# Kernel tuning notes

Measured on AMD Instinct MI355X. Metric: run time of the kernel, lower is better.

Reference implementation:

```python
import jax, jax.numpy as jnp
import numpy as np

N_PARENT = 16384
N_CHILD = 8 * N_PARENT  # nearest upsample, nempty=False: 8 children per parent
C = 128
K = 27  # 3x3x3 octree conv stencil


def setup_inputs() -> dict:
    key = jax.random.key(0)
    k1, k2, k3, k4 = jax.random.split(key, 4)
    x = jax.random.normal(k1, (N_PARENT, C), dtype=jnp.float32)
    # conv weight per stencil offset, fan-in scaled init
    w = jax.random.normal(k2, (K, C, C), dtype=jnp.float32) / np.sqrt(K * C)
    b = jnp.zeros((C,), dtype=jnp.float32)
    # neighbor table at depth+1; -1 marks missing neighbors (zero-padded)
    neigh = jax.random.randint(k3, (N_CHILD, K), -1, N_CHILD, dtype=jnp.int32)
    return {"x": x, "w": w, "b": b, "neigh": neigh}


def reference(x, w, b, neigh):
    # OctreeUpsample(nearest, nempty=False): copy each parent feature to its
    # 8 contiguous children at depth+1.
    xu = jnp.repeat(x, 8, axis=0)  # [N_child, C]
    # OctreeConv: gather 27 neighbors (missing -> 0), then GEMM + bias.
    valid = neigh >= 0  # [N_child, 27]
    g = jnp.where(valid[..., None], xu[jnp.clip(neigh, 0)], 0.0)  # [N_child, 27, C]
    out = jnp.einsum('nkc,kcd->nd', g, w) + b  # [N_child, C]
    return out
```

## Files before the change

kernel.cpp:

```cpp
#include <hip/hip_runtime.h>
#include <hip/hip_bf16.h>

#define N_PARENT 16384
#define N_CHILD (8 * N_PARENT)
#define CC 128
#define KK 27

#define BM 128
#define BN 128
#define BK 32

#define XB_OFF 0
#define XB_ELEMS (N_PARENT * CC)
#define WT_OFF XB_ELEMS
#define WT_ELEMS (KK * CC * CC)
#define ZR_OFF (WT_OFF + WT_ELEMS)
#define ZR_ELEMS 128
#define ZR_ROW 19840

typedef __attribute__((ext_vector_type(8))) __bf16 bf16x8;
typedef __attribute__((ext_vector_type(4))) float f32x4;

__device__ __forceinline__ void gll16(const void* g, void* l) {
  __builtin_amdgcn_global_load_lds(
      (const __attribute__((address_space(1))) unsigned int*)g,
      (__attribute__((address_space(3))) unsigned int*)l,
      16, 0, 0);
}

__global__ void prep_kernel(const float* __restrict__ x,
                            const float* __restrict__ w,
                            __hip_bfloat16* __restrict__ ws) {
  const int stride = gridDim.x * blockDim.x;
  const int tid = blockIdx.x * blockDim.x + threadIdx.x;
  for (int i = tid; i < XB_ELEMS; i += stride)
    ws[XB_OFF + i] = __float2bfloat16(x[i]);
  for (int j = tid; j < WT_ELEMS; j += stride) {
    const int k = j / (CC * CC);
    const int rem = j - k * CC * CC;
    const int d = rem >> 7;
    const int c = rem & 127;
    ws[WT_OFF + j] = __float2bfloat16(w[k * CC * CC + c * CC + d]);
  }
  if (tid < ZR_ELEMS) ws[ZR_OFF + tid] = __float2bfloat16(0.0f);
}

__global__ __launch_bounds__(256, 4) void upconv_kernel(
    const int* __restrict__ neigh,
    const __hip_bfloat16* __restrict__ ws,
    const float* __restrict__ bias,
    float* __restrict__ out) {
  __shared__ __align__(16) __hip_bfloat16 As[2][BM * BK];
  __shared__ __align__(16) __hip_bfloat16 Bs[2][BN * BK];
  __shared__ unsigned short ridx[BM * KK];

  const int tid = threadIdx.x;
  const int wv = tid >> 6;
  const int l = tid & 63;
  const int wr = wv >> 1;
  const int wc = wv & 1;
  const int row0 = blockIdx.x * BM;

  for (int j = tid; j < BM * KK; j += 256) {
    const int nv = neigh[row0 * KK + j];
    ridx[j] = (unsigned short)((nv >= 0) ? (nv >> 3) : ZR_ROW);
  }
  __syncthreads();

  const int lr = l & 15;
  const int lk8 = (l >> 4) * 8;
  const int g16 = l >> 2;
  const int lbA = (l & 3) * 16;
  const int sB = g16 * 256 + lbA;

  const char* xbB = (const char*)(ws + XB_OFF);
  const char* wp = (const char*)(ws + WT_OFF);

  f32x4 acc[4][4] = {};

  const int ri0 = (wv * 32 + g16) * KK;
  const int ri1 = (wv * 32 + 16 + g16) * KK;
  int r0 = ((int)ridx[ri0]) << 8;
  int r1 = ((int)ridx[ri1]) << 8;

  auto stageA = [&](int buf, int qb, int a0, int a1) {
    gll16(xbB + a0 + qb + lbA, &As[buf][(wv * 32) * BK]);
    gll16(xbB + a1 + qb + lbA, &As[buf][(wv * 32 + 16) * BK]);
  };
  auto stageB = [&](int buf, const char* w, int qb) {
    gll16(w + (wv * 32) * 256 + qb + sB, &Bs[buf][(wv * 32) * BK]);
    gll16(w + (wv * 32 + 16) * 256 + qb + sB, &Bs[buf][(wv * 32 + 16) * BK]);
  };

  auto compute = [&](int buf) {
    bf16x8 a[4], b[4];
#pragma unroll
    for (int m = 0; m < 4; ++m)
      a[m] = *reinterpret_cast<const bf16x8*>(
          &As[buf][(wr * 64 + m * 16 + lr) * BK + lk8]);
#pragma unroll
    for (int n = 0; n < 4; ++n)
      b[n] = *reinterpret_cast<const bf16x8*>(
          &Bs[buf][(wc * 64 + n * 16 + lr) * BK + lk8]);
    __builtin_amdgcn_s_setprio(1);
#pragma unroll
    for (int m = 0; m < 4; ++m)
#pragma unroll
      for (int n = 0; n < 4; ++n)
        acc[m][n] = __builtin_amdgcn_mfma_f32_16x16x32_bf16(
            a[m], b[n], acc[m][n], 0, 0, 0);
    __builtin_amdgcn_s_setprio(0);
  };

#define WAITN(n) asm volatile("s_waitcnt vmcnt(" #n ")" ::: "memory")
#define BAR() __builtin_amdgcn_s_barrier()

  stageB(0, wp, 0);
  stageA(0, 0, r0, r1);

  for (int k = 0; k < KK; ++k) {
    stageB(1, wp, 64);
    stageA(1, 64, r0, r1);
    WAITN(4); BAR();
    compute(0);
    BAR();

    stageB(0, wp, 128);
    stageA(0, 128, r0, r1);
    WAITN(4); BAR();
    compute(1);
    BAR();

    stageB(1, wp, 192);
    stageA(1, 192, r0, r1);
    int n0 = r0, n1 = r1;
    if (k + 1 < KK) {
      n0 = ((int)ridx[ri0 + k + 1]) << 8;
      n1 = ((int)ridx[ri1 + k + 1]) << 8;
    }
    WAITN(4); BAR();
    compute(0);
    BAR();

    wp += 2 * CC * CC;
    if (k + 1 < KK) {
      stageB(0, wp, 0);
      stageA(0, 0, n0, n1);
      WAITN(4);
    } else {
      WAITN(0);
    }
    BAR();
    compute(1);
    BAR();

    r0 = n0; r1 = n1;
  }

  float bv[4];
#pragma unroll
  for (int n = 0; n < 4; ++n) bv[n] = bias[wc * 64 + n * 16 + lr];
  const int rbase = row0 + wr * 64 + (l >> 4) * 4;
#pragma unroll
  for (int m = 0; m < 4; ++m)
#pragma unroll
    for (int n = 0; n < 4; ++n)
#pragma unroll
      for (int q = 0; q < 4; ++q)
        out[(size_t)(rbase + m * 16 + q) * CC + wc * 64 + n * 16 + lr] =
            acc[m][n][q] + bv[n];
}

extern "C" void kernel_launch(void* const* d_in, const int* in_sizes, int n_in,
                              void* d_out, int out_size, void* d_ws,
                              size_t ws_size, hipStream_t stream) {
  const float* x = (const float*)d_in[0];
  const float* w = (const float*)d_in[1];
  const float* b = (const float*)d_in[2];
  const int* neigh = (const int*)d_in[3];
  __hip_bfloat16* ws = (__hip_bfloat16*)d_ws;
  float* out = (float*)d_out;

  hipLaunchKernelGGL(prep_kernel, dim3(512), dim3(256), 0, stream, x, w, ws);
  hipLaunchKernelGGL(upconv_kernel, dim3(N_CHILD / BM), dim3(256), 0, stream,
                     neigh, ws, b, out);
}
```

Measured before the change: 152.2 us.

## Double M tile to 256 rows and XOR-swizzle LDS layout for gathers

Doubles the block's row tile from 128 to 256 so each wave holds a 128x64 accumulator (8x4 MFMA tiles), which halves the weight-tile loads per output row. Adds an XOR swizzle to both the global-to-LDS load lane offsets and the LDS fragment reads, intended to cut LDS bank conflicts. The vmcnt waits are adjusted to match the six async loads now issued per stage. In exchange, register pressure roughly doubles, launch bounds drop to 2 blocks per SM, and the grid halves, which lowers occupancy and reduces the number of blocks available to fill the CUs.

```diff
diff --git a/kernel.cpp b/kernel.cpp
--- a/kernel.cpp
+++ b/kernel.cpp
@@ -6,7 +6,7 @@
 #define CC 128
 #define KK 27
 
-#define BM 128
+#define BM 256
 #define BN 128
 #define BK 32
 
@@ -45,7 +45,7 @@
   if (tid < ZR_ELEMS) ws[ZR_OFF + tid] = __float2bfloat16(0.0f);
 }
 
-__global__ __launch_bounds__(256, 4) void upconv_kernel(
+__global__ __launch_bounds__(256, 2) void upconv_kernel(
     const int* __restrict__ neigh,
     const __hip_bfloat16* __restrict__ ws,
     const float* __restrict__ bias,
@@ -68,43 +68,44 @@
   __syncthreads();
 
   const int lr = l & 15;
-  const int lk8 = (l >> 4) * 8;
-  const int g16 = l >> 2;
-  const int lbA = (l & 3) * 16;
-  const int sB = g16 * 256 + lbA;
+  const int coE = (((l >> 4) ^ ((lr >> 1) & 3)) * 8);
+  const int lch = ((l & 3) ^ ((l >> 3) & 3)) * 16;
 
   const char* xbB = (const char*)(ws + XB_OFF);
-  const char* wp = (const char*)(ws + WT_OFF);
+  const char* wLane =
+      (const char*)(ws + WT_OFF) + (wv * 32 + (l >> 2)) * 256 + lch;
 
-  f32x4 acc[4][4] = {};
+  f32x4 acc[8][4] = {};
 
-  const int ri0 = (wv * 32 + g16) * KK;
-  const int ri1 = (wv * 32 + 16 + g16) * KK;
-  int r0 = ((int)ridx[ri0]) << 8;
-  int r1 = ((int)ridx[ri1]) << 8;
+  const int riB = (wv * 64 + (l >> 2)) * KK;
+  int rr[4], nr[4];
+#pragma unroll
+  for (int i = 0; i < 4; ++i) rr[i] = ((int)ridx[riB + i * 16 * KK]) << 8;
 
-  auto stageA = [&](int buf, int qb, int a0, int a1) {
-    gll16(xbB + a0 + qb + lbA, &As[buf][(wv * 32) * BK]);
-    gll16(xbB + a1 + qb + lbA, &As[buf][(wv * 32 + 16) * BK]);
+  auto stageA = [&](int buf, int qb, const int* r) {
+#pragma unroll
+    for (int i = 0; i < 4; ++i)
+      gll16(xbB + r[i] + qb + lch, &As[buf][(wv * 64 + i * 16) * BK]);
   };
-  auto stageB = [&](int buf, const char* w, int qb) {
-    gll16(w + (wv * 32) * 256 + qb + sB, &Bs[buf][(wv * 32) * BK]);
-    gll16(w + (wv * 32 + 16) * 256 + qb + sB, &Bs[buf][(wv * 32 + 16) * BK]);
+  auto stageB = [&](int buf, int tqb) {
+#pragma unroll
+    for (int j = 0; j < 2; ++j)
+      gll16(wLane + tqb + j * 4096, &Bs[buf][(wv * 32 + j * 16) * BK]);
   };
 
   auto compute = [&](int buf) {
-    bf16x8 a[4], b[4];
+    bf16x8 a[8], b[4];
 #pragma unroll
-    for (int m = 0; m < 4; ++m)
+    for (int m = 0; m < 8; ++m)
       a[m] = *reinterpret_cast<const bf16x8*>(
-          &As[buf][(wr * 64 + m * 16 + lr) * BK + lk8]);
+          &As[buf][(wr * 128 + m * 16 + lr) * BK + coE]);
 #pragma unroll
     for (int n = 0; n < 4; ++n)
       b[n] = *reinterpret_cast<const bf16x8*>(
-          &Bs[buf][(wc * 64 + n * 16 + lr) * BK + lk8]);
+          &Bs[buf][(wc * 64 + n * 16 + lr) * BK + coE]);
     __builtin_amdgcn_s_setprio(1);
 #pragma unroll
-    for (int m = 0; m < 4; ++m)
+    for (int m = 0; m < 8; ++m)
 #pragma unroll
       for (int n = 0; n < 4; ++n)
         acc[m][n] = __builtin_amdgcn_mfma_f32_16x16x32_bf16(
@@ -115,38 +116,38 @@
 #define WAITN(n) asm volatile("s_waitcnt vmcnt(" #n ")" ::: "memory")
 #define BAR() __builtin_amdgcn_s_barrier()
 
-  stageB(0, wp, 0);
-  stageA(0, 0, r0, r1);
+  stageB(0, 0);
+  stageA(0, 0, rr);
 
   for (int k = 0; k < KK; ++k) {
-    stageB(1, wp, 64);
-    stageA(1, 64, r0, r1);
-    WAITN(4); BAR();
+    const int tb = k * 32768;
+
+    stageB(1, tb + 64);
+    stageA(1, 64, rr);
+    WAITN(6); BAR();
     compute(0);
     BAR();
 
-    stageB(0, wp, 128);
-    stageA(0, 128, r0, r1);
-    WAITN(4); BAR();
+    stageB(0, tb + 128);
+    stageA(0, 128, rr);
+    WAITN(6); BAR();
     compute(1);
     BAR();
 
-    stageB(1, wp, 192);
-    stageA(1, 192, r0, r1);
-    int n0 = r0, n1 = r1;
-    if (k + 1 < KK) {
-      n0 = ((int)ridx[ri0 + k + 1]) << 8;
-      n1 = ((int)ridx[ri1 + k + 1]) << 8;
-    }
-    WAITN(4); BAR();
+    stageB(1, tb + 192);
+    stageA(1, 192, rr);
+#pragma unroll
+    for (int i = 0; i < 4; ++i)
+      nr[i] = (k + 1 < KK) ? (((int)ridx[riB + i * 16 * KK + k + 1]) << 8)
+                           : rr[i];
+    WAITN(6); BAR();
     compute(0);
     BAR();
 
-    wp += 2 * CC * CC;
     if (k + 1 < KK) {
-      stageB(0, wp, 0);
-      stageA(0, 0, n0, n1);
-      WAITN(4);
+      stageB(0, tb + 32768);
+      stageA(0, 0, nr);
+      WAITN(6);
     } else {
       WAITN(0);
     }
@@ -154,15 +155,16 @@
     compute(1);
     BAR();
 
-    r0 = n0; r1 = n1;
+#pragma unroll
+    for (int i = 0; i < 4; ++i) rr[i] = nr[i];
   }
 
   float bv[4];
 #pragma unroll
   for (int n = 0; n < 4; ++n) bv[n] = bias[wc * 64 + n * 16 + lr];
-  const int rbase = row0 + wr * 64 + (l >> 4) * 4;
+  const int rbase = row0 + wr * 128 + (l >> 4) * 4;
 #pragma unroll
-  for (int m = 0; m < 4; ++m)
+  for (int m = 0; m < 8; ++m)
 #pragma unroll
     for (int n = 0; n < 4; ++n)
 #pragma unroll
```

Measured after the change: 129.5 us. -14.9%, faster.
